# Optimization experiments

Hardware: AMD Instinct MI355X
Metric: run time of the kernel (lower is better)

Reference implementation:

```python
import jax, jax.numpy as jnp
import numpy as np

EMBED_DIM = 1024
NUM_HEADS = 16
HEAD_DIM = EMBED_DIM // NUM_HEADS
B, S = 2, 2048


def setup_inputs() -> dict:
    key = jax.random.key(0)
    ks = jax.random.split(key, 5)
    scale = 1.0 / np.sqrt(EMBED_DIM)
    return {
        "inputs": jax.random.normal(ks[0], (B, S, EMBED_DIM), dtype=jnp.float32),
        "Wq": jax.random.normal(ks[1], (EMBED_DIM, EMBED_DIM), dtype=jnp.float32) * scale,
        "bq": jnp.zeros((EMBED_DIM,), dtype=jnp.float32),
        "Wk": jax.random.normal(ks[2], (EMBED_DIM, EMBED_DIM), dtype=jnp.float32) * scale,
        "bk": jnp.zeros((EMBED_DIM,), dtype=jnp.float32),
        "Wv": jax.random.normal(ks[3], (EMBED_DIM, EMBED_DIM), dtype=jnp.float32) * scale,
        "bv": jnp.zeros((EMBED_DIM,), dtype=jnp.float32),
        "Wo": jax.random.normal(ks[4], (EMBED_DIM, EMBED_DIM), dtype=jnp.float32) * scale,
        "bo": jnp.zeros((EMBED_DIM,), dtype=jnp.float32),
    }


def _split_heads(x):
    # [B, S, E] -> [B, H, S, Dh]
    b, s, _ = x.shape
    return x.reshape(b, s, NUM_HEADS, HEAD_DIM).transpose(0, 2, 1, 3)


def reference(inputs, Wq, bq, Wk, bk, Wv, bv, Wo, bo):
    q = _split_heads(inputs @ Wq + bq)  # [B, H, S, Dh]
    k = _split_heads(inputs @ Wk + bk)
    v = _split_heads(inputs @ Wv + bv)
    scale = 1.0 / jnp.sqrt(jnp.asarray(HEAD_DIM, dtype=q.dtype))
    scores = jnp.einsum("bhqd,bhkd->bhqk", q, k) * scale  # [B, H, S, S]
    weights = jax.nn.softmax(scores, axis=-1)
    attn = jnp.einsum("bhqk,bhkd->bhqd", weights, v)  # [B, H, S, Dh]
    concat = attn.transpose(0, 2, 1, 3).reshape(inputs.shape[0], -1, EMBED_DIM)
    return concat @ Wo + bo
```

## Files before the change

### kernel.cpp

```cpp
#include <hip/hip_runtime.h>


#define QSCALE 0.18033688011112042f

using bf16x8 = __attribute__((ext_vector_type(8))) short;
using f32x16 = __attribute__((ext_vector_type(16))) float;
using u16x8  = __attribute__((ext_vector_type(8))) unsigned short;

__device__ __forceinline__ unsigned short f2bf(float f) {
  unsigned int u = __float_as_uint(f);
  u += 0x7fffu + ((u >> 16) & 1u);
  return (unsigned short)(u >> 16);
}

__device__ __forceinline__ void gload_lds16(const unsigned short* g, unsigned short* l) {
  __builtin_amdgcn_global_load_lds(
      (const __attribute__((address_space(1))) unsigned int*)g,
      (__attribute__((address_space(3))) unsigned int*)l, 16, 0, 0);
}

__global__ void conv_prep_kernel(const float* __restrict__ x, unsigned short* __restrict__ y,
                                 const float* __restrict__ W0, const float* __restrict__ W1,
                                 const float* __restrict__ W2, const float* __restrict__ W3,
                                 unsigned short* __restrict__ out) {
  __shared__ float t[32][33];
  int blk = blockIdx.x;
  if (blk >= 4096) {
    int i = (blk - 4096) * 256 + threadIdx.x;
    const float4* xf = (const float4*)x;
    float4 a = xf[i * 2], b = xf[i * 2 + 1];
    u16x8 o;
    o[0] = f2bf(a.x); o[1] = f2bf(a.y); o[2] = f2bf(a.z); o[3] = f2bf(a.w);
    o[4] = f2bf(b.x); o[5] = f2bf(b.y); o[6] = f2bf(b.z); o[7] = f2bf(b.w);
    *((u16x8*)y + i) = o;
    return;
  }
  int z = blk >> 10, rem = blk & 1023;
  const float* W = (z == 0) ? W0 : (z == 1) ? W1 : (z == 2) ? W2 : W3;
  unsigned short* o = out + (size_t)z * 1024 * 1024;
  int kt = (rem >> 5) * 32, nt = (rem & 31) * 32;
  int tx = threadIdx.x & 31, ty = threadIdx.x >> 5;
#pragma unroll
  for (int i = 0; i < 4; ++i)
    t[ty + i * 8][tx] = W[(size_t)(kt + ty + i * 8) * 1024 + nt + tx];
  __syncthreads();
#pragma unroll
  for (int i = 0; i < 4; ++i)
    o[(size_t)(nt + ty + i * 8) * 1024 + kt + tx] = f2bf(t[tx][ty + i * 8]);
}

__global__ __launch_bounds__(256) void gemm_bt_kernel(
    const unsigned short* __restrict__ A, const unsigned short* __restrict__ Bt,
    int mode, const float* __restrict__ bias0, const float* __restrict__ bias1,
    const float* __restrict__ bias2, unsigned short* __restrict__ Qh,
    unsigned short* __restrict__ Kh, unsigned short* __restrict__ Vt,
    float* __restrict__ Out) {
  const int K = 1024;
  __shared__ unsigned short SMEM[16384];

  int id = blockIdx.y * gridDim.x + blockIdx.x;
  int xcd = id & 7, pos = id >> 3;
  int bxr = pos >> 2, byr = xcd * 4 + (pos & 3);
  int n0 = bxr * 128, m0 = byr * 128;
  int tid = threadIdx.x;
  int w = tid >> 6, lane = tid & 63, l31 = lane & 31, half = lane >> 5;
  int wm = w >> 1, wn = w & 1;

  f32x16 acc[2][2];
#pragma unroll
  for (int i = 0; i < 2; ++i)
#pragma unroll
    for (int j = 0; j < 2; ++j)
#pragma unroll
      for (int r = 0; r < 16; ++r) acc[i][j][r] = 0.f;

  int srow = lane >> 2;
  int gchunk = (lane & 3) ^ ((srow >> 1) & 3);
  const unsigned short* Ag = A + (size_t)(m0 + 32 * w + srow) * K + gchunk * 8;
  const unsigned short* Bg = Bt + (size_t)(n0 + 32 * w + srow) * K + gchunk * 8;
  unsigned short* Asw = &SMEM[w * 1024];
  unsigned short* Bsw = &SMEM[8192 + w * 1024];

#pragma unroll
  for (int j = 0; j < 2; ++j) {
    gload_lds16(Ag + (size_t)(16 * j) * K, Asw + j * 512);
    gload_lds16(Bg + (size_t)(16 * j) * K, Bsw + j * 512);
  }

  for (int it = 0; it < 32; ++it) {
    int cur = (it & 1) * 4096;
    __syncthreads();
    if (it + 1 < 32) {
      int nxt = ((it + 1) & 1) * 4096;
      int kk = (it + 1) * 32;
#pragma unroll
      for (int j = 0; j < 2; ++j) {
        gload_lds16(Ag + kk + (size_t)(16 * j) * K, Asw + nxt + j * 512);
        gload_lds16(Bg + kk + (size_t)(16 * j) * K, Bsw + nxt + j * 512);
      }
    }
    const unsigned short* Asl = &SMEM[cur];
    const unsigned short* Bsl = &SMEM[8192 + cur];
#pragma unroll
    for (int kc = 0; kc < 2; ++kc) {
      int swk = (l31 >> 1) & 3;
      int ph = ((kc * 2 + half) ^ swk) * 8;
      bf16x8 af[2], bfr[2];
#pragma unroll
      for (int mt = 0; mt < 2; ++mt)
        af[mt] = *(bf16x8*)&Asl[(wm * 64 + mt * 32 + l31) * 32 + ph];
#pragma unroll
      for (int nt = 0; nt < 2; ++nt)
        bfr[nt] = *(bf16x8*)&Bsl[(wn * 64 + nt * 32 + l31) * 32 + ph];
#pragma unroll
      for (int mt = 0; mt < 2; ++mt)
#pragma unroll
        for (int nt = 0; nt < 2; ++nt)
          acc[mt][nt] = __builtin_amdgcn_mfma_f32_32x32x16_bf16(af[mt], bfr[nt], acc[mt][nt], 0, 0, 0);
    }
  }

  if (mode == 1) {
#pragma unroll
    for (int mt = 0; mt < 2; ++mt)
#pragma unroll
      for (int nt = 0; nt < 2; ++nt)
#pragma unroll
        for (int r = 0; r < 16; ++r) {
          int row = (r & 3) + 8 * (r >> 2) + 4 * half;
          int gm = m0 + wm * 64 + mt * 32 + row;
          int gn = n0 + wn * 64 + nt * 32 + l31;
          Out[(size_t)gm * 1024 + gn] = acc[mt][nt][r] + bias0[gn];
        }
    return;
  }

  int btype = bxr >> 3;
  if (btype < 2) {
    const float* bp = btype ? bias1 : bias0;
    unsigned short* dst = btype ? Kh : Qh;
    float sc = btype ? 1.0f : QSCALE;
#pragma unroll
    for (int mt = 0; mt < 2; ++mt)
#pragma unroll
      for (int nt = 0; nt < 2; ++nt)
#pragma unroll
        for (int r = 0; r < 16; ++r) {
          int row = (r & 3) + 8 * (r >> 2) + 4 * half;
          int gm = m0 + wm * 64 + mt * 32 + row;
          int gn = n0 + wn * 64 + nt * 32 + l31;
          int e = gn & 1023;
          float v = (acc[mt][nt][r] + bp[e]) * sc;
          int hh = e >> 6, d = e & 63;
          int bb = gm >> 11, s = gm & 2047;
          dst[(((size_t)(bb * 16 + hh)) * 2048 + s) * 64 + d] = f2bf(v);
        }
  } else {
    __syncthreads();
    unsigned short* T = SMEM;
#pragma unroll
    for (int mt = 0; mt < 2; ++mt)
#pragma unroll
      for (int nt = 0; nt < 2; ++nt)
#pragma unroll
        for (int r = 0; r < 16; ++r) {
          int row = (r & 3) + 8 * (r >> 2) + 4 * half;
          int sl = wm * 64 + mt * 32 + row;
          int dl = wn * 64 + nt * 32 + l31;
          int e = (n0 - 2048) + dl;
          float v = acc[mt][nt][r] + bias2[e];
          T[dl * 128 + (sl ^ ((dl & 15) << 3))] = f2bf(v);
        }
    __syncthreads();
    int bb = m0 >> 11, s0 = m0 & 2047;
    int h0 = (n0 - 2048) >> 6;
    int rr0 = tid >> 2, csub = tid & 3;
#pragma unroll
    for (int pass = 0; pass < 2; ++pass) {
      int rr = rr0 + 64 * pass;
      int hh = h0 + (rr >> 6), d = rr & 63;
      unsigned short* vrow = Vt + (((size_t)(bb * 16 + hh)) * 64 + d) * 2048 + s0;
#pragma unroll
      for (int c = 0; c < 4; ++c) {
        int cc = c * 4 + csub;
        uint4 val = *(uint4*)&T[rr * 128 + ((cc ^ (rr & 15)) * 8)];
        *(uint4*)&vrow[cc * 8] = val;
      }
    }
  }
}

__global__ __launch_bounds__(512, 1) void attn_kernel(
    const unsigned short* __restrict__ Qh, const unsigned short* __restrict__ Kh,
    const unsigned short* __restrict__ Vt, unsigned short* __restrict__ Ctx) {
  __shared__ __align__(16) unsigned short SM[65536];

  int bx = blockIdx.x;
  int xcd = bx & 7, tt = bx >> 3;
  int qt = tt & 7;
  int bhi = (tt >> 3) * 8 + xcd;
  int h = bhi & 15, b = bhi >> 4;

  int tid = threadIdx.x;
  int w = tid >> 6, lane = tid & 63, l31 = lane & 31, half = lane >> 5;
  int l7 = l31 & 7;
  int mw = w & 3, kw = w >> 2;

  size_t bh = (size_t)bhi;
  const unsigned short* Qb  = Qh + (bh * 2048 + (size_t)qt * 256) * 64;
  const unsigned short* Kbh = Kh + bh * 131072;
  const unsigned short* Vbh = Vt + bh * 131072;

  bf16x8 qf0[4], qf1[4];
#pragma unroll
  for (int kc = 0; kc < 4; ++kc) {
    qf0[kc] = *(const bf16x8*)&Qb[(size_t)(mw * 64 + l31) * 64 + kc * 16 + half * 8];
    qf1[kc] = *(const bf16x8*)&Qb[(size_t)(mw * 64 + 32 + l31) * 64 + kc * 16 + half * 8];
  }

  int r8 = lane >> 3, gc = (lane & 7) ^ r8;
  int t = w >> 1, s0 = (w & 1) * 4;
  const unsigned short* gb[4];
  int lofs[4];
  int gstep;
#pragma unroll
  for (int j = 0; j < 4; ++j) {
    int s = s0 + j;
    if (t < 2) { gb[j] = Kbh + (size_t)(t * 1024 + s * 8 + r8) * 64 + gc * 8; }
    else       { gb[j] = Vbh + (size_t)(s * 8 + r8) * 2048 + (t - 2) * 1024 + gc * 8; }
    lofs[j] = t * 4096 + s * 512;
  }
  gstep = (t < 2) ? 4096 : 64;

#pragma unroll
  for (int j = 0; j < 4; ++j) { gload_lds16(gb[j], SM + lofs[j]); gb[j] += gstep; }
#pragma unroll
  for (int j = 0; j < 4; ++j) { gload_lds16(gb[j], SM + 16384 + lofs[j]); gb[j] += gstep; }

  f32x16 o00, o01, o10, o11;
#pragma unroll
  for (int r = 0; r < 16; ++r) { o00[r] = 0.f; o01[r] = 0.f; o10[r] = 0.f; o11[r] = 0.f; }
  float l0 = 0.f, l1 = 0.f;

  for (int i = 0; i < 16; ++i) {
    if ((i & 1) == 0) __syncthreads();
    if (i + 2 < 16) {
      unsigned short* nb = SM + (((i + 2) & 3) << 14);
#pragma unroll
      for (int j = 0; j < 4; ++j) { gload_lds16(gb[j], nb + lofs[j]); gb[j] += gstep; }
    }
    const unsigned short* cur = SM + ((i & 3) << 14);
    const unsigned short* Ksw = cur + kw * 4096;
    const unsigned short* Vsw = cur + 8192 + kw * 4096;

    f32x16 s00, s01, s10, s11;
#pragma unroll
    for (int r = 0; r < 16; ++r) { s00[r] = 0.f; s01[r] = 0.f; s10[r] = 0.f; s11[r] = 0.f; }
    __builtin_amdgcn_s_setprio(1);
#pragma unroll
    for (int kc = 0; kc < 4; ++kc) {
      int ph = ((kc * 2 + half) ^ l7) * 8;
      bf16x8 kb0 = *(bf16x8*)&Ksw[l31 * 64 + ph];
      bf16x8 kb1 = *(bf16x8*)&Ksw[(32 + l31) * 64 + ph];
      s00 = __builtin_amdgcn_mfma_f32_32x32x16_bf16(kb0, qf0[kc], s00, 0, 0, 0);
      s01 = __builtin_amdgcn_mfma_f32_32x32x16_bf16(kb1, qf0[kc], s01, 0, 0, 0);
      s10 = __builtin_amdgcn_mfma_f32_32x32x16_bf16(kb0, qf1[kc], s10, 0, 0, 0);
      s11 = __builtin_amdgcn_mfma_f32_32x32x16_bf16(kb1, qf1[kc], s11, 0, 0, 0);
    }
    __builtin_amdgcn_s_setprio(0);

    bf16x8 U0[4], U1[4];
    auto smx = [&](const f32x16& sa, const f32x16& sb, float& lacc, bf16x8* U) {
      float pa[16], pb[16];
#pragma unroll
      for (int r = 0; r < 16; ++r) {
        pa[r] = __builtin_amdgcn_exp2f(sa[r]);
        pb[r] = __builtin_amdgcn_exp2f(sb[r]);
      }
      float t0 = 0.f, t1 = 0.f, t2 = 0.f, t3 = 0.f;
#pragma unroll
      for (int r = 0; r < 16; r += 4) {
        t0 += pa[r] + pb[r]; t1 += pa[r + 1] + pb[r + 1];
        t2 += pa[r + 2] + pb[r + 2]; t3 += pa[r + 3] + pb[r + 3];
      }
      lacc += (t0 + t1) + (t2 + t3);
      unsigned int own[16];
#pragma unroll
      for (int m = 0; m < 4; ++m)
#pragma unroll
        for (int p = 0; p < 2; ++p) {
          int r = 4 * m + 2 * p;
          unsigned int wa, wb;
          asm("v_cvt_pk_bf16_f32 %0, %1, %2" : "=v"(wa) : "v"(pa[r]), "v"(pa[r + 1]));
          asm("v_cvt_pk_bf16_f32 %0, %1, %2" : "=v"(wb) : "v"(pb[r]), "v"(pb[r + 1]));
          own[2 * m + p] = wa;
          own[2 * m + 8 + p] = wb;
        }
#pragma unroll
      for (int kc = 0; kc < 4; ++kc) {
        unsigned int a0 = own[4 * kc],     b0 = own[4 * kc + 2];
        unsigned int a1 = own[4 * kc + 1], b1 = own[4 * kc + 3];
        asm("v_permlane32_swap_b32 %0, %1" : "+v"(a0), "+v"(b0));
        asm("v_permlane32_swap_b32 %0, %1" : "+v"(a1), "+v"(b1));
        union { unsigned int u[4]; bf16x8 v; } Uu;
        Uu.u[0] = a0; Uu.u[1] = a1; Uu.u[2] = b0; Uu.u[3] = b1;
        U[kc] = Uu.v;
      }
    };
    smx(s00, s01, l0, U0);
    smx(s10, s11, l1, U1);

    __builtin_amdgcn_s_setprio(1);
#pragma unroll
    for (int kc = 0; kc < 4; ++kc) {
      int ph = ((kc * 2 + half) ^ l7) * 8;
      bf16x8 vb0 = *(bf16x8*)&Vsw[l31 * 64 + ph];
      bf16x8 vb1 = *(bf16x8*)&Vsw[(32 + l31) * 64 + ph];
      o00 = __builtin_amdgcn_mfma_f32_32x32x16_bf16(U0[kc], vb0, o00, 0, 0, 0);
      o01 = __builtin_amdgcn_mfma_f32_32x32x16_bf16(U0[kc], vb1, o01, 0, 0, 0);
      o10 = __builtin_amdgcn_mfma_f32_32x32x16_bf16(U1[kc], vb0, o10, 0, 0, 0);
      o11 = __builtin_amdgcn_mfma_f32_32x32x16_bf16(U1[kc], vb1, o11, 0, 0, 0);
    }
    __builtin_amdgcn_s_setprio(0);
  }

  float lw0 = l0 + __shfl_xor(l0, 32);
  float lw1 = l1 + __shfl_xor(l1, 32);
  __syncthreads();
  float* mrgO = (float*)SM;
  float* mrgL = (float*)SM + 8192;
  int slot2 = (mw & 1) * 2;
  int phase = mw >> 1;
#pragma unroll
  for (int p = 0; p < 2; ++p) {
    if (kw == 1 && phase == p) {
      auto dump = [&](const f32x16& a0, const f32x16& a1, float lw, int qg) {
        float* dst = mrgO + (slot2 + qg) * 2048 + lane * 32;
#pragma unroll
        for (int c = 0; c < 8; ++c) {
          float4 t4;
          if (c < 4) t4 = make_float4(a0[4 * c], a0[4 * c + 1], a0[4 * c + 2], a0[4 * c + 3]);
          else       t4 = make_float4(a1[4 * (c - 4)], a1[4 * (c - 4) + 1], a1[4 * (c - 4) + 2], a1[4 * (c - 4) + 3]);
          *(float4*)&dst[(c ^ l7) * 4] = t4;
        }
        if (half == 0) mrgL[(slot2 + qg) * 32 + l31] = lw;
      };
      dump(o00, o01, lw0, 0);
      dump(o10, o11, lw1, 1);
    }
    __syncthreads();
    if (kw == 0 && phase == p) {
      auto fin = [&](f32x16& a0, f32x16& a1, float lw, int qg) {
        const float* src = mrgO + (slot2 + qg) * 2048 + lane * 32;
#pragma unroll
        for (int c = 0; c < 8; ++c) {
          float4 t4 = *(const float4*)&src[(c ^ l7) * 4];
          if (c < 4) { a0[4 * c] += t4.x; a0[4 * c + 1] += t4.y; a0[4 * c + 2] += t4.z; a0[4 * c + 3] += t4.w; }
          else       { a1[4 * (c - 4)] += t4.x; a1[4 * (c - 4) + 1] += t4.y; a1[4 * (c - 4) + 2] += t4.z; a1[4 * (c - 4) + 3] += t4.w; }
        }
        lw += mrgL[(slot2 + qg) * 32 + l31];
        float inv = 1.0f / lw;
#pragma unroll
        for (int r = 0; r < 16; ++r) {
          int rmap = (r & 3) + 8 * (r >> 2) + 4 * half;
          float invr = __shfl(inv, rmap);
          size_t row = (size_t)(b * 2048 + qt * 256 + mw * 64 + qg * 32 + rmap);
          Ctx[row * 1024 + h * 64 + l31]      = f2bf(a0[r] * invr);
          Ctx[row * 1024 + h * 64 + 32 + l31] = f2bf(a1[r] * invr);
        }
      };
      fin(o00, o01, lw0, 0);
      fin(o10, o11, lw1, 1);
    }
    __syncthreads();
  }
}

extern "C" void kernel_launch(void* const* d_in, const int* in_sizes, int n_in,
                              void* d_out, int out_size, void* d_ws, size_t ws_size,
                              hipStream_t stream) {
  const float* X  = (const float*)d_in[0];
  const float* Wq = (const float*)d_in[1];
  const float* bq = (const float*)d_in[2];
  const float* Wk = (const float*)d_in[3];
  const float* bk = (const float*)d_in[4];
  const float* Wv = (const float*)d_in[5];
  const float* bv = (const float*)d_in[6];
  const float* Wo = (const float*)d_in[7];
  const float* bo = (const float*)d_in[8];

  if (ws_size < (size_t)48 * 1024 * 1024) return;

  char* ws = (char*)d_ws;
  unsigned short* Xbf = (unsigned short*)(ws);
  unsigned short* Wt  = (unsigned short*)(ws + ((size_t)8 << 20));
  unsigned short* Qh  = (unsigned short*)(ws + ((size_t)16 << 20));
  unsigned short* Kh  = (unsigned short*)(ws + ((size_t)24 << 20));
  unsigned short* Vt  = (unsigned short*)(ws + ((size_t)32 << 20));
  unsigned short* Ctx = (unsigned short*)(ws + ((size_t)40 << 20));
  unsigned short* WtO = Wt + (size_t)3 * 1024 * 1024;

  conv_prep_kernel<<<6144, 256, 0, stream>>>(X, Xbf, Wq, Wk, Wv, Wo, Wt);
  gemm_bt_kernel<<<dim3(24, 32), 256, 0, stream>>>(Xbf, Wt, 0, bq, bk, bv, Qh, Kh, Vt, nullptr);
  attn_kernel<<<dim3(256), 512, 0, stream>>>(Qh, Kh, Vt, Ctx);
  gemm_bt_kernel<<<dim3(8, 32), 256, 0, stream>>>(Ctx, WtO, 1, bo, bo, bo, nullptr, nullptr, nullptr, (float*)d_out);
}
```

Before: 187.5 us.

## Software-pipeline QK^T/softmax of next tile with PV of previous tile

Restructures the attention main loop so that the QK^T product and exp/pack for tile i are issued before the PV product for tile i-1. Two P-fragment register sets alternate between iterations, and LDS prefetch and barriers are placed once per tile. The goal is to overlap the VALU softmax work with MFMA work from a different tile. Launch bounds also move to 2 blocks per CU. That caps the register budget while the extra P buffers raise register pressure, so spills are possible, and the 128KB LDS per block probably still blocks a second resident block.

```diff
diff --git a/kernel.cpp b/kernel.cpp
--- a/kernel.cpp
+++ b/kernel.cpp
@@ -190,7 +190,7 @@
   }
 }
 
-__global__ __launch_bounds__(512, 1) void attn_kernel(
+__global__ __launch_bounds__(512, 2) void attn_kernel(
     const unsigned short* __restrict__ Qh, const unsigned short* __restrict__ Kh,
     const unsigned short* __restrict__ Vt, unsigned short* __restrict__ Ctx) {
   __shared__ __align__(16) unsigned short SM[65536];
@@ -232,27 +232,53 @@
   }
   gstep = (t < 2) ? 4096 : 64;
 
-#pragma unroll
-  for (int j = 0; j < 4; ++j) { gload_lds16(gb[j], SM + lofs[j]); gb[j] += gstep; }
-#pragma unroll
-  for (int j = 0; j < 4; ++j) { gload_lds16(gb[j], SM + 16384 + lofs[j]); gb[j] += gstep; }
-
   f32x16 o00, o01, o10, o11;
 #pragma unroll
   for (int r = 0; r < 16; ++r) { o00[r] = 0.f; o01[r] = 0.f; o10[r] = 0.f; o11[r] = 0.f; }
   float l0 = 0.f, l1 = 0.f;
 
-  for (int i = 0; i < 16; ++i) {
-    if ((i & 1) == 0) __syncthreads();
-    if (i + 2 < 16) {
-      unsigned short* nb = SM + (((i + 2) & 3) << 14);
-#pragma unroll
-      for (int j = 0; j < 4; ++j) { gload_lds16(gb[j], nb + lofs[j]); gb[j] += gstep; }
-    }
-    const unsigned short* cur = SM + ((i & 3) << 14);
-    const unsigned short* Ksw = cur + kw * 4096;
-    const unsigned short* Vsw = cur + 8192 + kw * 4096;
-
+  bf16x8 UA0[4], UA1[4], UB0[4], UB1[4];
+
+  auto smx = [&](const f32x16& sa, const f32x16& sb, float& lacc, bf16x8* U) {
+    float pa[16], pb[16];
+#pragma unroll
+    for (int r = 0; r < 16; ++r) {
+      pa[r] = __builtin_amdgcn_exp2f(sa[r]);
+      pb[r] = __builtin_amdgcn_exp2f(sb[r]);
+    }
+    float t0 = 0.f, t1 = 0.f, t2 = 0.f, t3 = 0.f;
+#pragma unroll
+    for (int r = 0; r < 16; r += 4) {
+      t0 += pa[r] + pb[r]; t1 += pa[r + 1] + pb[r + 1];
+      t2 += pa[r + 2] + pb[r + 2]; t3 += pa[r + 3] + pb[r + 3];
+    }
+    lacc += (t0 + t1) + (t2 + t3);
+    unsigned int own[16];
+#pragma unroll
+    for (int m = 0; m < 4; ++m)
+#pragma unroll
+      for (int p = 0; p < 2; ++p) {
+        int r = 4 * m + 2 * p;
+        unsigned int wa, wb;
+        asm("v_cvt_pk_bf16_f32 %0, %1, %2" : "=v"(wa) : "v"(pa[r]), "v"(pa[r + 1]));
+        asm("v_cvt_pk_bf16_f32 %0, %1, %2" : "=v"(wb) : "v"(pb[r]), "v"(pb[r + 1]));
+        own[2 * m + p] = wa;
+        own[2 * m + 8 + p] = wb;
+      }
+#pragma unroll
+    for (int kc = 0; kc < 4; ++kc) {
+      unsigned int a0 = own[4 * kc],     b0 = own[4 * kc + 2];
+      unsigned int a1 = own[4 * kc + 1], b1 = own[4 * kc + 3];
+      asm("v_permlane32_swap_b32 %0, %1" : "+v"(a0), "+v"(b0));
+      asm("v_permlane32_swap_b32 %0, %1" : "+v"(a1), "+v"(b1));
+      union { unsigned int u[4]; bf16x8 v; } Uu;
+      Uu.u[0] = a0; Uu.u[1] = a1; Uu.u[2] = b0; Uu.u[3] = b1;
+      U[kc] = Uu.v;
+    }
+  };
+
+  auto qktsmx = [&](int i, bf16x8* U0, bf16x8* U1) {
+    const unsigned short* Ksw = SM + ((i & 3) << 14) + kw * 4096;
     f32x16 s00, s01, s10, s11;
 #pragma unroll
     for (int r = 0; r < 16; ++r) { s00[r] = 0.f; s01[r] = 0.f; s10[r] = 0.f; s11[r] = 0.f; }
@@ -268,48 +294,12 @@
       s11 = __builtin_amdgcn_mfma_f32_32x32x16_bf16(kb1, qf1[kc], s11, 0, 0, 0);
     }
     __builtin_amdgcn_s_setprio(0);
-
-    bf16x8 U0[4], U1[4];
-    auto smx = [&](const f32x16& sa, const f32x16& sb, float& lacc, bf16x8* U) {
-      float pa[16], pb[16];
-#pragma unroll
-      for (int r = 0; r < 16; ++r) {
-        pa[r] = __builtin_amdgcn_exp2f(sa[r]);
-        pb[r] = __builtin_amdgcn_exp2f(sb[r]);
-      }
-      float t0 = 0.f, t1 = 0.f, t2 = 0.f, t3 = 0.f;
-#pragma unroll
-      for (int r = 0; r < 16; r += 4) {
-        t0 += pa[r] + pb[r]; t1 += pa[r + 1] + pb[r + 1];
-        t2 += pa[r + 2] + pb[r + 2]; t3 += pa[r + 3] + pb[r + 3];
-      }
-      lacc += (t0 + t1) + (t2 + t3);
-      unsigned int own[16];
-#pragma unroll
-      for (int m = 0; m < 4; ++m)
-#pragma unroll
-        for (int p = 0; p < 2; ++p) {
-          int r = 4 * m + 2 * p;
-          unsigned int wa, wb;
-          asm("v_cvt_pk_bf16_f32 %0, %1, %2" : "=v"(wa) : "v"(pa[r]), "v"(pa[r + 1]));
-          asm("v_cvt_pk_bf16_f32 %0, %1, %2" : "=v"(wb) : "v"(pb[r]), "v"(pb[r + 1]));
-          own[2 * m + p] = wa;
-          own[2 * m + 8 + p] = wb;
-        }
-#pragma unroll
-      for (int kc = 0; kc < 4; ++kc) {
-        unsigned int a0 = own[4 * kc],     b0 = own[4 * kc + 2];
-        unsigned int a1 = own[4 * kc + 1], b1 = own[4 * kc + 3];
-        asm("v_permlane32_swap_b32 %0, %1" : "+v"(a0), "+v"(b0));
-        asm("v_permlane32_swap_b32 %0, %1" : "+v"(a1), "+v"(b1));
-        union { unsigned int u[4]; bf16x8 v; } Uu;
-        Uu.u[0] = a0; Uu.u[1] = a1; Uu.u[2] = b0; Uu.u[3] = b1;
-        U[kc] = Uu.v;
-      }
-    };
     smx(s00, s01, l0, U0);
     smx(s10, s11, l1, U1);
-
+  };
+
+  auto pv = [&](int i, const bf16x8* U0, const bf16x8* U1) {
+    const unsigned short* Vsw = SM + ((i & 3) << 14) + 8192 + kw * 4096;
     __builtin_amdgcn_s_setprio(1);
 #pragma unroll
     for (int kc = 0; kc < 4; ++kc) {
@@ -322,7 +312,40 @@
       o11 = __builtin_amdgcn_mfma_f32_32x32x16_bf16(U1[kc], vb1, o11, 0, 0, 0);
     }
     __builtin_amdgcn_s_setprio(0);
-  }
+  };
+
+  auto prefetch = [&](int tile) {
+    if (tile < 16) {
+      unsigned short* nb = SM + ((tile & 3) << 14);
+#pragma unroll
+      for (int j = 0; j < 4; ++j) { gload_lds16(gb[j], nb + lofs[j]); gb[j] += gstep; }
+    }
+  };
+
+#pragma unroll
+  for (int j = 0; j < 4; ++j) { gload_lds16(gb[j], SM + lofs[j]); gb[j] += gstep; }
+#pragma unroll
+  for (int j = 0; j < 4; ++j) { gload_lds16(gb[j], SM + 16384 + lofs[j]); gb[j] += gstep; }
+  __syncthreads();
+  prefetch(2);
+  qktsmx(0, UA0, UA1);
+
+  for (int ip = 0; ip < 7; ++ip) {
+    int i1 = 2 * ip + 1;
+    __syncthreads();
+    prefetch(i1 + 2);
+    qktsmx(i1, UB0, UB1);
+    pv(i1 - 1, UA0, UA1);
+    int i2 = i1 + 1;
+    __syncthreads();
+    prefetch(i2 + 2);
+    qktsmx(i2, UA0, UA1);
+    pv(i2 - 1, UB0, UB1);
+  }
+  __syncthreads();
+  qktsmx(15, UB0, UB1);
+  pv(14, UA0, UA1);
+  pv(15, UB0, UB1);
 
   float lw0 = l0 + __shfl_xor(l0, 32);
   float lw1 = l1 + __shfl_xor(l1, 32);
```

Result: slower. 209.5 us (+11.7%).
